# Performance work log

Measured on AMD Instinct MI355X. Metric: run time of the kernel, lower is better.

## Reference

```python
import jax, jax.numpy as jnp
import numpy as np
import math

EMB = 768
B, S = 8, 2048

def setup_inputs() -> dict:
    key = jax.random.key(0)
    ks = jax.random.split(key, 6)
    q = jax.random.normal(ks[0], (B, S, EMB), dtype=jnp.float32)
    k = jax.random.normal(ks[1], (B, S, EMB), dtype=jnp.float32)
    v = jax.random.normal(ks[2], (B, S, EMB), dtype=jnp.float32)
    mask = jax.random.randint(ks[3], (B, S, S), 0, 2, dtype=jnp.int32)
    # nn.Linear(emb, emb): weight [out, in], bias [out]
    bound = 1.0 / math.sqrt(EMB)
    W = jax.random.uniform(ks[4], (EMB, EMB), minval=-bound, maxval=bound, dtype=jnp.float32)
    b = jax.random.uniform(ks[5], (EMB,), minval=-bound, maxval=bound, dtype=jnp.float32)
    return {"q": q, "k": k, "v": v, "mask": mask, "W": W, "b": b}

def reference(q, k, v, mask, W, b):
    # shared linear projection (torch Linear: x @ W^T + b)
    qp = jnp.einsum('bse,oe->bso', q, W) + b
    kp = jnp.einsum('bse,oe->bso', k, W) + b
    vp = jnp.einsum('bse,oe->bso', v, W) + b
    scores = jnp.einsum('bqe,bke->bqk', qp, kp) / math.sqrt(EMB)  # [B,S,S]
    scores = jnp.where(mask == 1, -jnp.inf, scores)
    attn = jax.nn.softmax(scores, axis=-1)
    return jnp.einsum('bqk,bke->bqe', attn, vp)
```

## Files before the change

kernel.cpp:

```cpp
#include <hip/hip_runtime.h>
#include <hip/hip_bf16.h>
#include <stdint.h>

#define B_ 8
#define S_ 2048
#define E_ 768

typedef __attribute__((ext_vector_type(4))) float f32x4;
typedef __attribute__((ext_vector_type(8))) short bf16x8;


__device__ __forceinline__ unsigned pk2bf(float x, float y) {
  unsigned r;
  asm("v_cvt_pk_bf16_f32 %0, %1, %2" : "=v"(r) : "v"(x), "v"(y));
  return r;
}

__device__ __forceinline__ void gll16(const void* g, void* l) {
  __builtin_amdgcn_global_load_lds((const __attribute__((address_space(1))) void*)g,
                                   (__attribute__((address_space(3))) void*)l, 16, 0, 0);
}

__device__ __forceinline__ void gemm128(const char* __restrict__ Ab,
                                        const char* __restrict__ Bb,
                                        int ldA, int ldB, int NT,
                                        unsigned short* As, unsigned short* Bs,
                                        int tid, int wm, int wn, int lane,
                                        f32x4 (&acc)[4][4]) {
  unsigned sA[2], sB[2], lin2[2];
#pragma unroll
  for (int i = 0; i < 2; ++i) {
    const unsigned lin = (unsigned)i * 4096u + (unsigned)tid * 16u;
    const unsigned row = lin >> 6, ch = (lin >> 4) & 3u;
    const unsigned sw = (ch ^ ((row >> 1) & 3u)) << 4;
    sA[i] = row * (unsigned)ldA + sw;
    sB[i] = row * (unsigned)ldB + sw;
    lin2[i] = lin;
  }
  unsigned aoff[4], boff[4];
#pragma unroll
  for (int m = 0; m < 4; ++m) {
    unsigned row = (unsigned)(wm * 64 + m * 16 + (lane & 15));
    aoff[m] = row * 64 + ((((unsigned)lane >> 4) ^ ((row >> 1) & 3u)) << 4);
    row = (unsigned)(wn * 64 + m * 16 + (lane & 15));
    boff[m] = row * 64 + ((((unsigned)lane >> 4) ^ ((row >> 1) & 3u)) << 4);
  }
#pragma unroll
  for (int i = 0; i < 2; ++i) {
    gll16(Ab + sA[i], (char*)As + lin2[i]);
    gll16(Bb + sB[i], (char*)Bs + lin2[i]);
  }
#pragma unroll
  for (int i = 0; i < 2; ++i) {
    gll16(Ab + sA[i] + 64, (char*)As + 8192 + lin2[i]);
    gll16(Bb + sB[i] + 64, (char*)Bs + 8192 + lin2[i]);
  }
  asm volatile("s_waitcnt vmcnt(4)" ::: "memory");
  __builtin_amdgcn_s_barrier();
  __builtin_amdgcn_sched_barrier(0);
  for (int kt = 0; kt < NT; ++kt) {
    const int bc = kt % 3;
    const char* Ac = (const char*)As + bc * 8192;
    const char* Bc = (const char*)Bs + bc * 8192;
    if (kt + 2 < NT) {
      const int bn = (kt + 2) % 3;
      const size_t ko = (size_t)(kt + 2) * 64;
#pragma unroll
      for (int i = 0; i < 2; ++i) {
        gll16(Ab + sA[i] + ko, (char*)As + bn * 8192 + lin2[i]);
        gll16(Bb + sB[i] + ko, (char*)Bs + bn * 8192 + lin2[i]);
      }
    }
    bf16x8 af[4], bf[4];
#pragma unroll
    for (int m = 0; m < 4; ++m) af[m] = *reinterpret_cast<const bf16x8*>(Ac + aoff[m]);
#pragma unroll
    for (int n = 0; n < 4; ++n) bf[n] = *reinterpret_cast<const bf16x8*>(Bc + boff[n]);
    asm volatile("s_waitcnt lgkmcnt(0)" ::: "memory");
    __builtin_amdgcn_sched_barrier(0);
    __builtin_amdgcn_s_setprio(1);
#pragma unroll
    for (int m = 0; m < 4; ++m)
#pragma unroll
      for (int n = 0; n < 4; ++n)
        acc[m][n] = __builtin_amdgcn_mfma_f32_16x16x32_bf16(af[m], bf[n], acc[m][n], 0, 0, 0);
    __builtin_amdgcn_s_setprio(0);
    if (kt + 1 < NT) {
      if (kt + 2 < NT) asm volatile("s_waitcnt vmcnt(4)" ::: "memory");
      else             asm volatile("s_waitcnt vmcnt(0)" ::: "memory");
      __builtin_amdgcn_s_barrier();
      __builtin_amdgcn_sched_barrier(0);
    }
  }
}

__global__ __launch_bounds__(256) void k_cvt(const float* __restrict__ q,
                                             const float* __restrict__ k,
                                             const float* __restrict__ v,
                                             const float* __restrict__ W,
                                             const int* __restrict__ mask,
                                             unsigned short* __restrict__ qb,
                                             unsigned short* __restrict__ kb,
                                             unsigned short* __restrict__ vb,
                                             unsigned short* __restrict__ Wb,
                                             unsigned long long* __restrict__ mwords) {
  const int y = blockIdx.y;
  if (y == 3) {
    const int nchunks = B_ * S_ * (S_ / 256);
    const int lane = threadIdx.x & 63;
    const int wave = (blockIdx.x * 256 + threadIdx.x) >> 6;
    const int nw = gridDim.x * 4;
    int c = wave;
    for (; c + 3 * nw < nchunks; c += 4 * nw) {
      int4 v0 = *reinterpret_cast<const int4*>(&mask[(size_t)c * 256 + lane * 4]);
      int4 v1 = *reinterpret_cast<const int4*>(&mask[(size_t)(c + nw) * 256 + lane * 4]);
      int4 v2 = *reinterpret_cast<const int4*>(&mask[(size_t)(c + 2 * nw) * 256 + lane * 4]);
      int4 v3 = *reinterpret_cast<const int4*>(&mask[(size_t)(c + 3 * nw) * 256 + lane * 4]);
      unsigned long long a0 = __ballot(v0.x == 1), a1 = __ballot(v0.y == 1);
      unsigned long long a2 = __ballot(v0.z == 1), a3 = __ballot(v0.w == 1);
      unsigned long long b0 = __ballot(v1.x == 1), b1 = __ballot(v1.y == 1);
      unsigned long long b2 = __ballot(v1.z == 1), b3 = __ballot(v1.w == 1);
      unsigned long long c0 = __ballot(v2.x == 1), c1 = __ballot(v2.y == 1);
      unsigned long long c2 = __ballot(v2.z == 1), c3 = __ballot(v2.w == 1);
      unsigned long long d0 = __ballot(v3.x == 1), d1 = __ballot(v3.y == 1);
      unsigned long long d2 = __ballot(v3.z == 1), d3 = __ballot(v3.w == 1);
      if (lane == 0) {
        *reinterpret_cast<ulonglong2*>(&mwords[(size_t)c * 4]) = make_ulonglong2(a0, a1);
        *reinterpret_cast<ulonglong2*>(&mwords[(size_t)c * 4 + 2]) = make_ulonglong2(a2, a3);
        *reinterpret_cast<ulonglong2*>(&mwords[(size_t)(c + nw) * 4]) = make_ulonglong2(b0, b1);
        *reinterpret_cast<ulonglong2*>(&mwords[(size_t)(c + nw) * 4 + 2]) = make_ulonglong2(b2, b3);
        *reinterpret_cast<ulonglong2*>(&mwords[(size_t)(c + 2 * nw) * 4]) = make_ulonglong2(c0, c1);
        *reinterpret_cast<ulonglong2*>(&mwords[(size_t)(c + 2 * nw) * 4 + 2]) = make_ulonglong2(c2, c3);
        *reinterpret_cast<ulonglong2*>(&mwords[(size_t)(c + 3 * nw) * 4]) = make_ulonglong2(d0, d1);
        *reinterpret_cast<ulonglong2*>(&mwords[(size_t)(c + 3 * nw) * 4 + 2]) = make_ulonglong2(d2, d3);
      }
    }
    for (; c < nchunks; c += nw) {
      int4 v0 = *reinterpret_cast<const int4*>(&mask[(size_t)c * 256 + lane * 4]);
      unsigned long long a0 = __ballot(v0.x == 1), a1 = __ballot(v0.y == 1);
      unsigned long long a2 = __ballot(v0.z == 1), a3 = __ballot(v0.w == 1);
      if (lane == 0) {
        *reinterpret_cast<ulonglong2*>(&mwords[(size_t)c * 4]) = make_ulonglong2(a0, a1);
        *reinterpret_cast<ulonglong2*>(&mwords[(size_t)c * 4 + 2]) = make_ulonglong2(a2, a3);
      }
    }
    return;
  }
  if (y == 4) {
    if (blockIdx.x < 288) {
      const int i0 = blockIdx.x * 512 + threadIdx.x;
      const float4* s4 = reinterpret_cast<const float4*>(W);
      uint2* d2 = reinterpret_cast<uint2*>(Wb);
      float4 f0 = s4[i0];
      float4 f1 = s4[i0 + 256];
      d2[i0]       = make_uint2(pk2bf(f0.x, f0.y), pk2bf(f0.z, f0.w));
      d2[i0 + 256] = make_uint2(pk2bf(f1.x, f1.y), pk2bf(f1.z, f1.w));
    }
    return;
  }
  const float* src = (y == 0) ? q : (y == 1) ? k : v;
  unsigned short* dst = (y == 0) ? qb : (y == 1) ? kb : vb;
  const int i0 = blockIdx.x * 512 + threadIdx.x;
  const float4* s4 = reinterpret_cast<const float4*>(src);
  uint2* d2 = reinterpret_cast<uint2*>(dst);
  float4 f0 = s4[i0];
  float4 f1 = s4[i0 + 256];
  d2[i0]       = make_uint2(pk2bf(f0.x, f0.y), pk2bf(f0.z, f0.w));
  d2[i0 + 256] = make_uint2(pk2bf(f1.x, f1.y), pk2bf(f1.z, f1.w));
}

__global__ __launch_bounds__(256, 3) void k_projb(const unsigned short* __restrict__ Xb,
                                                  const unsigned short* __restrict__ Wb,
                                                  const float* __restrict__ bias,
                                                  unsigned short* __restrict__ qp,
                                                  unsigned short* __restrict__ kp,
                                                  unsigned short* __restrict__ vp) {
  __shared__ __attribute__((aligned(16))) unsigned short As[3 * 4096];
  __shared__ __attribute__((aligned(16))) unsigned short Bs[3 * 4096];
  const int tid = threadIdx.x, lane = tid & 63, wid = tid >> 6;
  const int wm = wid >> 1, wn = wid & 1;
  const int id = blockIdx.x;
  const int swz = (id & 7) * 288 + (id >> 3);
  const int z = swz / 768;
  const int rem = swz - z * 768;
  const int r0 = (rem / 6) * 128, c0 = (rem % 6) * 128;
  const unsigned short* X = Xb + (size_t)z * (B_ * S_ * E_);
  unsigned short* O = (z == 0) ? qp : ((z == 1) ? kp : vp);

  f32x4 acc[4][4] = {};
  gemm128((const char*)(X + (size_t)r0 * E_), (const char*)(Wb + (size_t)c0 * E_),
          E_ * 2, E_ * 2, E_ / 32, As, Bs, tid, wm, wn, lane, acc);

  float bcol[4];
#pragma unroll
  for (int n = 0; n < 4; ++n) bcol[n] = bias[c0 + wn * 64 + n * 16 + (lane & 15)];
#pragma unroll
  for (int m = 0; m < 4; ++m)
#pragma unroll
    for (int r = 0; r < 4; ++r) {
      const int row = r0 + wm * 64 + m * 16 + (lane >> 4) * 4 + r;
#pragma unroll
      for (int n = 0; n < 4; ++n) {
        const int col = c0 + wn * 64 + n * 16 + (lane & 15);
        O[(size_t)row * E_ + col] = (unsigned short)pk2bf(acc[m][n][r] + bcol[n], 0.f);
      }
    }
}

__global__ __launch_bounds__(256, 3) void k_scores(const unsigned short* __restrict__ qp,
                                                   const unsigned short* __restrict__ kp,
                                                   const unsigned long long* __restrict__ mwords,
                                                   unsigned short* __restrict__ P,
                                                   float* __restrict__ rowsum,
                                                   const unsigned short* __restrict__ vp,
                                                   unsigned short* __restrict__ vpT) {
  __shared__ __attribute__((aligned(16))) unsigned short SM[25088];
  unsigned short* As = SM;
  unsigned short* Bs = SM + 12288;
  float* rlds = (float*)(SM + 24576);
  const int tid = threadIdx.x, lane = tid & 63, wid = tid >> 6;
  if (blockIdx.x < 3072) {
    unsigned short (*t)[72] = (unsigned short (*)[72])SM;
    const int id = blockIdx.x;
    const int st = id & 31;
    const int ot = (id >> 5) % 12;
    const int b = id / 384;
#pragma unroll
    for (int i = 0; i < 2; ++i) {
      int f = i * 256 + tid;
      int s = f >> 3, c8 = f & 7;
      uint4 vv = *reinterpret_cast<const uint4*>(
          &vp[((size_t)b * S_ + st * 64 + s) * E_ + ot * 64 + c8 * 8]);
      *reinterpret_cast<uint4*>(&t[s][c8 * 8]) = vv;
    }
    __syncthreads();
    const int o = tid >> 2;
    const int sb = (tid & 3) * 16;
    unsigned p[8];
#pragma unroll
    for (int j = 0; j < 8; ++j)
      p[j] = (unsigned)t[sb + 2 * j][o] | ((unsigned)t[sb + 2 * j + 1][o] << 16);
    uint4 w0 = make_uint4(p[0], p[1], p[2], p[3]);
    uint4 w1 = make_uint4(p[4], p[5], p[6], p[7]);
    size_t ob = ((size_t)b * E_ + ot * 64 + o) * S_ + st * 64 + sb;
    *reinterpret_cast<uint4*>(&vpT[ob]) = w0;
    *reinterpret_cast<uint4*>(&vpT[ob + 8]) = w1;
    return;
  }
  const int wm = wid >> 1, wn = wid & 1;
  const int id = blockIdx.x - 3072;
  const int swz = (id & 7) * 256 + (id >> 3);
  const int b = swz >> 8;
  const int qt = (swz >> 4) & 15, yt = swz & 15;
  f32x4 acc[4][4] = {};
  gemm128((const char*)(qp + ((size_t)b * S_ + qt * 128) * E_),
          (const char*)(kp + ((size_t)b * S_ + yt * 128) * E_),
          E_ * 2, E_ * 2, E_ / 32, As, Bs, tid, wm, wn, lane, acc);

  const float SC = (float)(1.4426950408889634 / 27.712812921102035);
#pragma unroll
  for (int m = 0; m < 4; ++m)
#pragma unroll
    for (int r = 0; r < 4; ++r) {
      const int rloc = wm * 64 + m * 16 + (lane >> 4) * 4 + r;
      const int grow = qt * 128 + rloc;
      const size_t rowoff = ((size_t)b * S_ + grow) * S_;
      const unsigned long long mw =
          mwords[(((size_t)b * S_ + grow) * 8 + (yt >> 1)) * 4 + (lane & 3)];
      const int shb = (yt & 1) * 32 + wn * 16 + ((lane & 15) >> 2);
      const int cbase = yt * 128 + wn * 64 + (lane & 15);
      float radd = 0.f;
#pragma unroll
      for (int n = 0; n < 4; ++n) {
        float pv = ((mw >> (shb + n * 4)) & 1ull)
                       ? 0.f
                       : __builtin_amdgcn_exp2f(acc[m][n][r] * SC);
        radd += pv;
        P[rowoff + cbase + n * 16] = (unsigned short)pk2bf(pv, 0.f);
      }
      float vsum = radd;
      vsum += __shfl_xor(vsum, 1);
      vsum += __shfl_xor(vsum, 2);
      vsum += __shfl_xor(vsum, 4);
      vsum += __shfl_xor(vsum, 8);
      if ((lane & 15) == 0) rlds[rloc * 2 + wn] = vsum;
    }
  __syncthreads();
  if (tid < 128) {
    rowsum[(size_t)yt * (B_ * S_) + (size_t)b * S_ + qt * 128 + tid] =
        rlds[tid * 2] + rlds[tid * 2 + 1];
  }
}

__global__ __launch_bounds__(256) void k_invrs(const float* __restrict__ rowsum,
                                               float* __restrict__ inv_rs) {
  int i = blockIdx.x * 256 + threadIdx.x;
  float t = 0.f;
#pragma unroll
  for (int g = 0; g < 16; ++g) t += rowsum[(size_t)g * (B_ * S_) + i];
  inv_rs[i] = 1.0f / t;
}

__global__ __launch_bounds__(256, 3) void k_pv(const unsigned short* __restrict__ P,
                                               const unsigned short* __restrict__ vpT,
                                               const float* __restrict__ inv_rs,
                                               float* __restrict__ out) {
  __shared__ __attribute__((aligned(16))) unsigned short As[3 * 4096];
  __shared__ __attribute__((aligned(16))) unsigned short Bs[3 * 4096];
  const int tid = threadIdx.x, lane = tid & 63, wid = tid >> 6;
  const int wm = wid >> 1, wn = wid & 1;
  const int id = blockIdx.x;
  const int swz = (id & 7) * 96 + (id >> 3);
  const int b = swz / 96;
  const int rem = swz - b * 96;
  const int mt = rem / 6, et = rem % 6;
  f32x4 acc[4][4] = {};
  gemm128((const char*)(P + ((size_t)b * S_ + mt * 128) * S_),
          (const char*)(vpT + ((size_t)b * E_ + et * 128) * S_),
          S_ * 2, S_ * 2, S_ / 32, As, Bs, tid, wm, wn, lane, acc);

#pragma unroll
  for (int m = 0; m < 4; ++m)
#pragma unroll
    for (int r = 0; r < 4; ++r) {
      const int grow = mt * 128 + wm * 64 + m * 16 + (lane >> 4) * 4 + r;
      const float inv = inv_rs[b * S_ + grow];
#pragma unroll
      for (int n = 0; n < 4; ++n) {
        const int col = et * 128 + wn * 64 + n * 16 + (lane & 15);
        out[((size_t)b * S_ + grow) * E_ + col] = acc[m][n][r] * inv;
      }
    }
}

extern "C" void kernel_launch(void* const* d_in, const int* in_sizes, int n_in,
                              void* d_out, int out_size, void* d_ws, size_t ws_size,
                              hipStream_t stream) {
  const float* q = (const float*)d_in[0];
  const float* k = (const float*)d_in[1];
  const float* v = (const float*)d_in[2];
  const int* mask = (const int*)d_in[3];
  const float* W = (const float*)d_in[4];
  const float* bias = (const float*)d_in[5];
  float* out = (float*)d_out;
  char* ws = (char*)d_ws;

  unsigned short* qb = (unsigned short*)(ws + 0);
  unsigned short* kb = (unsigned short*)(ws + 25165824);
  unsigned short* vb = (unsigned short*)(ws + 50331648);
  unsigned short* Wb = (unsigned short*)(ws + 75497472);
  unsigned short* qp = (unsigned short*)(ws + 76677120);
  unsigned short* kp = (unsigned short*)(ws + 101842944);
  unsigned short* vpT = (unsigned short*)(ws + 127008768);
  unsigned short* P = (unsigned short*)(ws + 0);
  float* rowsum = (float*)(ws + 75497472);
  float* inv_rs = (float*)(ws + 76546048);
  unsigned short* vp_tmp = (unsigned short*)d_out;
  unsigned long long* mwords =
      (unsigned long long*)((char*)d_out + 25165824);
  (void)in_sizes; (void)n_in; (void)out_size; (void)ws_size;

  dim3 blk(256, 1, 1);
  k_cvt<<<dim3(6144, 5, 1), blk, 0, stream>>>(q, k, v, W, mask, qb, kb, vb, Wb, mwords);
  k_projb<<<dim3(2304, 1, 1), blk, 0, stream>>>(qb, Wb, bias, qp, kp, vp_tmp);
  k_scores<<<dim3(5120, 1, 1), blk, 0, stream>>>(qp, kp, mwords, P, rowsum, vp_tmp, vpT);
  k_invrs<<<dim3(64, 1, 1), blk, 0, stream>>>(rowsum, inv_rs);
  k_pv<<<dim3(768, 1, 1), blk, 0, stream>>>(P, vpT, inv_rs, out);
}
```

Before: 303.8 us.

## Fuse V transpose into projection epilogue and switch GEMM to double buffering

The V projection blocks now transpose their output tile through shared memory and write vpT directly. This removes the separate transpose blocks in the scores kernel and the round trip of vp through the output buffer. The shared GEMM loop drops from triple to double buffering, with a full vmcnt(0) wait each iteration, to cut LDS use and allow four blocks per CU. The cost is less load/compute overlap in every GEMM, since the next tile's fetch must finish before the barrier.

```diff
diff --git a/kernel.cpp b/kernel.cpp
--- a/kernel.cpp
+++ b/kernel.cpp
@@ -50,25 +50,20 @@
     gll16(Ab + sA[i], (char*)As + lin2[i]);
     gll16(Bb + sB[i], (char*)Bs + lin2[i]);
   }
-#pragma unroll
-  for (int i = 0; i < 2; ++i) {
-    gll16(Ab + sA[i] + 64, (char*)As + 8192 + lin2[i]);
-    gll16(Bb + sB[i] + 64, (char*)Bs + 8192 + lin2[i]);
-  }
-  asm volatile("s_waitcnt vmcnt(4)" ::: "memory");
+  asm volatile("s_waitcnt vmcnt(0)" ::: "memory");
   __builtin_amdgcn_s_barrier();
   __builtin_amdgcn_sched_barrier(0);
   for (int kt = 0; kt < NT; ++kt) {
-    const int bc = kt % 3;
-    const char* Ac = (const char*)As + bc * 8192;
-    const char* Bc = (const char*)Bs + bc * 8192;
-    if (kt + 2 < NT) {
-      const int bn = (kt + 2) % 3;
-      const size_t ko = (size_t)(kt + 2) * 64;
+    const char* Ac = (const char*)As + (kt & 1) * 8192;
+    const char* Bc = (const char*)Bs + (kt & 1) * 8192;
+    char* An = (char*)As + ((kt + 1) & 1) * 8192;
+    char* Bn = (char*)Bs + ((kt + 1) & 1) * 8192;
+    if (kt + 1 < NT) {
+      const size_t ko = (size_t)(kt + 1) * 64;
 #pragma unroll
       for (int i = 0; i < 2; ++i) {
-        gll16(Ab + sA[i] + ko, (char*)As + bn * 8192 + lin2[i]);
-        gll16(Bb + sB[i] + ko, (char*)Bs + bn * 8192 + lin2[i]);
+        gll16(Ab + sA[i] + ko, An + lin2[i]);
+        gll16(Bb + sB[i] + ko, Bn + lin2[i]);
       }
     }
     bf16x8 af[4], bf[4];
@@ -86,8 +81,7 @@
         acc[m][n] = __builtin_amdgcn_mfma_f32_16x16x32_bf16(af[m], bf[n], acc[m][n], 0, 0, 0);
     __builtin_amdgcn_s_setprio(0);
     if (kt + 1 < NT) {
-      if (kt + 2 < NT) asm volatile("s_waitcnt vmcnt(4)" ::: "memory");
-      else             asm volatile("s_waitcnt vmcnt(0)" ::: "memory");
+      asm volatile("s_waitcnt vmcnt(0)" ::: "memory");
       __builtin_amdgcn_s_barrier();
       __builtin_amdgcn_sched_barrier(0);
     }
@@ -169,14 +163,15 @@
   d2[i0 + 256] = make_uint2(pk2bf(f1.x, f1.y), pk2bf(f1.z, f1.w));
 }
 
-__global__ __launch_bounds__(256, 3) void k_projb(const unsigned short* __restrict__ Xb,
+__global__ __launch_bounds__(256, 4) void k_projb(const unsigned short* __restrict__ Xb,
                                                   const unsigned short* __restrict__ Wb,
                                                   const float* __restrict__ bias,
                                                   unsigned short* __restrict__ qp,
                                                   unsigned short* __restrict__ kp,
-                                                  unsigned short* __restrict__ vp) {
-  __shared__ __attribute__((aligned(16))) unsigned short As[3 * 4096];
-  __shared__ __attribute__((aligned(16))) unsigned short Bs[3 * 4096];
+                                                  unsigned short* __restrict__ vpT) {
+  __shared__ __attribute__((aligned(16))) unsigned short SM[16896];
+  unsigned short* As = SM;
+  unsigned short* Bs = SM + 8192;
   const int tid = threadIdx.x, lane = tid & 63, wid = tid >> 6;
   const int wm = wid >> 1, wn = wid & 1;
   const int id = blockIdx.x;
@@ -185,7 +180,6 @@
   const int rem = swz - z * 768;
   const int r0 = (rem / 6) * 128, c0 = (rem % 6) * 128;
   const unsigned short* X = Xb + (size_t)z * (B_ * S_ * E_);
-  unsigned short* O = (z == 0) ? qp : ((z == 1) ? kp : vp);
 
   f32x4 acc[4][4] = {};
   gemm128((const char*)(X + (size_t)r0 * E_), (const char*)(Wb + (size_t)c0 * E_),
@@ -194,6 +188,34 @@
   float bcol[4];
 #pragma unroll
   for (int n = 0; n < 4; ++n) bcol[n] = bias[c0 + wn * 64 + n * 16 + (lane & 15)];
+
+  if (z == 2) {
+    __syncthreads();
+#pragma unroll
+    for (int m = 0; m < 4; ++m)
+#pragma unroll
+      for (int r = 0; r < 4; ++r) {
+        const int row = wm * 64 + m * 16 + (lane >> 4) * 4 + r;
+#pragma unroll
+        for (int n = 0; n < 4; ++n) {
+          const int col = wn * 64 + n * 16 + (lane & 15);
+          SM[col * 132 + row] = (unsigned short)pk2bf(acc[m][n][r] + bcol[n], 0.f);
+        }
+      }
+    __syncthreads();
+    const int b = r0 >> 11;
+    const int s0 = r0 & 2047;
+#pragma unroll
+    for (int i = 0; i < 16; ++i) {
+      const int f = i * 256 + tid;
+      const int e = f >> 5, su = f & 31;
+      uint2 val = *reinterpret_cast<const uint2*>(&SM[e * 132 + su * 4]);
+      *reinterpret_cast<uint2*>(&vpT[((size_t)b * E_ + c0 + e) * S_ + s0 + su * 4]) = val;
+    }
+    return;
+  }
+
+  unsigned short* O = (z == 0) ? qp : kp;
 #pragma unroll
   for (int m = 0; m < 4; ++m)
 #pragma unroll
@@ -207,48 +229,18 @@
     }
 }
 
-__global__ __launch_bounds__(256, 3) void k_scores(const unsigned short* __restrict__ qp,
+__global__ __launch_bounds__(256, 4) void k_scores(const unsigned short* __restrict__ qp,
                                                    const unsigned short* __restrict__ kp,
                                                    const unsigned long long* __restrict__ mwords,
                                                    unsigned short* __restrict__ P,
-                                                   float* __restrict__ rowsum,
-                                                   const unsigned short* __restrict__ vp,
-                                                   unsigned short* __restrict__ vpT) {
-  __shared__ __attribute__((aligned(16))) unsigned short SM[25088];
+                                                   float* __restrict__ rowsum) {
+  __shared__ __attribute__((aligned(16))) unsigned short SM[16384];
   unsigned short* As = SM;
-  unsigned short* Bs = SM + 12288;
-  float* rlds = (float*)(SM + 24576);
+  unsigned short* Bs = SM + 8192;
+  float* rlds = (float*)SM;
   const int tid = threadIdx.x, lane = tid & 63, wid = tid >> 6;
-  if (blockIdx.x < 3072) {
-    unsigned short (*t)[72] = (unsigned short (*)[72])SM;
-    const int id = blockIdx.x;
-    const int st = id & 31;
-    const int ot = (id >> 5) % 12;
-    const int b = id / 384;
-#pragma unroll
-    for (int i = 0; i < 2; ++i) {
-      int f = i * 256 + tid;
-      int s = f >> 3, c8 = f & 7;
-      uint4 vv = *reinterpret_cast<const uint4*>(
-          &vp[((size_t)b * S_ + st * 64 + s) * E_ + ot * 64 + c8 * 8]);
-      *reinterpret_cast<uint4*>(&t[s][c8 * 8]) = vv;
-    }
-    __syncthreads();
-    const int o = tid >> 2;
-    const int sb = (tid & 3) * 16;
-    unsigned p[8];
-#pragma unroll
-    for (int j = 0; j < 8; ++j)
-      p[j] = (unsigned)t[sb + 2 * j][o] | ((unsigned)t[sb + 2 * j + 1][o] << 16);
-    uint4 w0 = make_uint4(p[0], p[1], p[2], p[3]);
-    uint4 w1 = make_uint4(p[4], p[5], p[6], p[7]);
-    size_t ob = ((size_t)b * E_ + ot * 64 + o) * S_ + st * 64 + sb;
-    *reinterpret_cast<uint4*>(&vpT[ob]) = w0;
-    *reinterpret_cast<uint4*>(&vpT[ob + 8]) = w1;
-    return;
-  }
   const int wm = wid >> 1, wn = wid & 1;
-  const int id = blockIdx.x - 3072;
+  const int id = blockIdx.x;
   const int swz = (id & 7) * 256 + (id >> 3);
   const int b = swz >> 8;
   const int qt = (swz >> 4) & 15, yt = swz & 15;
@@ -256,6 +248,7 @@
   gemm128((const char*)(qp + ((size_t)b * S_ + qt * 128) * E_),
           (const char*)(kp + ((size_t)b * S_ + yt * 128) * E_),
           E_ * 2, E_ * 2, E_ / 32, As, Bs, tid, wm, wn, lane, acc);
+  __syncthreads();
 
   const float SC = (float)(1.4426950408889634 / 27.712812921102035);
 #pragma unroll
@@ -301,12 +294,13 @@
   inv_rs[i] = 1.0f / t;
 }
 
-__global__ __launch_bounds__(256, 3) void k_pv(const unsigned short* __restrict__ P,
+__global__ __launch_bounds__(256, 4) void k_pv(const unsigned short* __restrict__ P,
                                                const unsigned short* __restrict__ vpT,
                                                const float* __restrict__ inv_rs,
                                                float* __restrict__ out) {
-  __shared__ __attribute__((aligned(16))) unsigned short As[3 * 4096];
-  __shared__ __attribute__((aligned(16))) unsigned short Bs[3 * 4096];
+  __shared__ __attribute__((aligned(16))) unsigned short SM[16384];
+  unsigned short* As = SM;
+  unsigned short* Bs = SM + 8192;
   const int tid = threadIdx.x, lane = tid & 63, wid = tid >> 6;
   const int wm = wid >> 1, wn = wid & 1;
   const int id = blockIdx.x;
@@ -355,15 +349,14 @@
   unsigned short* P = (unsigned short*)(ws + 0);
   float* rowsum = (float*)(ws + 75497472);
   float* inv_rs = (float*)(ws + 76546048);
-  unsigned short* vp_tmp = (unsigned short*)d_out;
   unsigned long long* mwords =
       (unsigned long long*)((char*)d_out + 25165824);
   (void)in_sizes; (void)n_in; (void)out_size; (void)ws_size;
 
   dim3 blk(256, 1, 1);
   k_cvt<<<dim3(6144, 5, 1), blk, 0, stream>>>(q, k, v, W, mask, qb, kb, vb, Wb, mwords);
-  k_projb<<<dim3(2304, 1, 1), blk, 0, stream>>>(qb, Wb, bias, qp, kp, vp_tmp);
-  k_scores<<<dim3(5120, 1, 1), blk, 0, stream>>>(qp, kp, mwords, P, rowsum, vp_tmp, vpT);
+  k_projb<<<dim3(2304, 1, 1), blk, 0, stream>>>(qb, Wb, bias, qp, kp, vpT);
+  k_scores<<<dim3(2048, 1, 1), blk, 0, stream>>>(qp, kp, mwords, P, rowsum);
   k_invrs<<<dim3(64, 1, 1), blk, 0, stream>>>(rowsum, inv_rs);
   k_pv<<<dim3(768, 1, 1), blk, 0, stream>>>(P, vpT, inv_rs, out);
 }
```

Result: faster. 287.2 us, median of 2 (-5.5%).
